# Kernel tuning notes

Measured on AMD Instinct MI355X. Metric: run time of the kernel, lower is better.

The kernel has to match this reference:

```python
import jax, jax.numpy as jnp
import numpy as np


def _warp(x, flow):
    """Bilinear backward warp (grid_sample, zeros padding, pixel coords).
    x: [B,C,H,W], flow: [B,2,H,W] with flow[:,0]=dx, flow[:,1]=dy."""
    B, C, H, W = x.shape
    gx = jnp.arange(W, dtype=x.dtype)[None, None, :] + flow[:, 0]  # [B,H,W]
    gy = jnp.arange(H, dtype=x.dtype)[None, :, None] + flow[:, 1]  # [B,H,W]
    x0 = jnp.floor(gx)
    y0 = jnp.floor(gy)
    wx = gx - x0
    wy = gy - y0
    x0 = x0.astype(jnp.int32)
    y0 = y0.astype(jnp.int32)
    xf = x.reshape(B, C, H * W)

    def tap(yi, xi, w):
        valid = (xi >= 0) & (xi < W) & (yi >= 0) & (yi < H)
        idx = (jnp.clip(yi, 0, H - 1) * W + jnp.clip(xi, 0, W - 1)).reshape(B, 1, H * W)
        v = jnp.take_along_axis(xf, idx, axis=2).reshape(B, C, H, W)
        return v * (w * valid)[:, None]

    return (tap(y0, x0, (1 - wx) * (1 - wy))
            + tap(y0, x0 + 1, wx * (1 - wy))
            + tap(y0 + 1, x0, (1 - wx) * wy)
            + tap(y0 + 1, x0 + 1, wx * wy))


def _shift(flow, bias):
    # shift(Flow, motion): warp the flow field itself by a constant motion vector
    B, _, H, W = flow.shape
    const = jnp.broadcast_to(jnp.asarray(bias, flow.dtype).reshape(1, 2, 1, 1), (B, 2, H, W))
    return _warp(flow, const)


def _make_obmc(x, flow):
    vols = [_warp(x, flow)]
    for bias in ([0.0, 1.0], [1.0, 0.0], [0.0, -1.0], [-1.0, 0.0]):
        vols.append(_warp(x, _shift(flow, bias)))
    return jnp.concatenate(vols, axis=1)  # [B, 5*C, H, W]


def setup_inputs() -> dict:
    key = jax.random.key(0)
    k1, k2 = jax.random.split(key)
    x = jax.random.normal(k1, (4, 64, 256, 256), dtype=jnp.float32)
    flow = jax.random.normal(k2, (4, 2, 256, 256), dtype=jnp.float32) * 4.0
    return {"x": x, "flow": flow}


def reference(x, flow):
    return _make_obmc(x, flow)
```

## Files before the change

kernel.cpp:

```cpp
#include <hip/hip_runtime.h>

#define BB 4
#define CC 64
#define HH 256
#define WW 256
#define HWHW (HH * WW)

__global__ __launch_bounds__(256) void transpose_xk(const float* __restrict__ x,
                                                    float* __restrict__ xt) {
    __shared__ float tile[64][65];
    const int b = blockIdx.y;
    const int hw0 = blockIdx.x << 6;
    const int t = threadIdx.x;
    const float* xb = x + (size_t)b * CC * HWHW;

    const int cq = t >> 4;
    const int px4 = (t & 15) << 2;
#pragma unroll
    for (int k = 0; k < 4; ++k) {
        const int c = cq + (k << 4);
        const float4 v = *(const float4*)&xb[(size_t)c * HWHW + hw0 + px4];
        tile[c][px4 + 0] = v.x;
        tile[c][px4 + 1] = v.y;
        tile[c][px4 + 2] = v.z;
        tile[c][px4 + 3] = v.w;
    }
    __syncthreads();
    float* xtb = xt + ((size_t)b * HWHW << 6);
    const int hwq = t >> 4;
    const int c4 = (t & 15) << 2;
#pragma unroll
    for (int k = 0; k < 4; ++k) {
        const int hw = hwq + (k << 4);
        float4 v;
        v.x = tile[c4 + 0][hw];
        v.y = tile[c4 + 1][hw];
        v.z = tile[c4 + 2][hw];
        v.w = tile[c4 + 3][hw];
        *(float4*)&xtb[((size_t)(hw0 + hw) << 6) + c4] = v;
    }
}

__global__ __launch_bounds__(256) void obmc_kernel(const float* __restrict__ xt,
                                                   const float* __restrict__ flow,
                                                   float* __restrict__ out) {
    __shared__ int4 dOff[5][64];
    __shared__ float4 dW[5][64];
    __shared__ float sm[64][65];

    const int bid = ((blockIdx.x & 7) << 9) + (blockIdx.x >> 3);
    const int tx0 = (bid & 3) << 6;
    const int y = (bid >> 2) & 255;
    const int b = bid >> 10;
    const int t = threadIdx.x;
    const int wv = t >> 6;
    const int lane = t & 63;
    const int sp = lane >> 4;
    const int c4 = (lane & 15) << 2;

    const float* xtb = xt + ((size_t)b * HWHW << 6);
    const float* fb = flow + (size_t)b * 2 * HWHW;
    float* ob = out + (size_t)b * 5 * CC * HWHW + (size_t)y * WW + tx0;

    const int oys[5] = {0, 1, 0, -1, 0};
    const int oxs[5] = {0, 0, 1, 0, -1};

    for (int idx = t; idx < 320; idx += 256) {
        const int g = idx >> 6, px = idx & 63;
        const int sy = y + oys[g];
        const int sx = tx0 + px + oxs[g];
        float fx = 0.f, fy = 0.f;
        if ((unsigned)sy < HH && (unsigned)sx < WW) {
            const int fo = sy * WW + sx;
            fx = fb[fo];
            fy = fb[HWHW + fo];
        }
        const float gx = (float)(tx0 + px) + fx;
        const float gy = (float)y + fy;
        const float x0f = floorf(gx);
        const float y0f = floorf(gy);
        const float fwx = gx - x0f;
        const float fwy = gy - y0f;
        const int ix0 = (int)x0f, iy0 = (int)y0f;
        const int ix1 = ix0 + 1, iy1 = iy0 + 1;
        const float vx0 = ((unsigned)ix0 < WW) ? 1.f : 0.f;
        const float vx1 = ((unsigned)ix1 < WW) ? 1.f : 0.f;
        const float vy0 = ((unsigned)iy0 < HH) ? 1.f : 0.f;
        const float vy1 = ((unsigned)iy1 < HH) ? 1.f : 0.f;
        const int xc0 = min(max(ix0, 0), WW - 1);
        const int xc1 = min(max(ix1, 0), WW - 1);
        const int yc0 = min(max(iy0, 0), HH - 1);
        const int yc1 = min(max(iy1, 0), HH - 1);
        dOff[g][px] = make_int4((yc0 * WW + xc0) << 6, (yc0 * WW + xc1) << 6,
                                (yc1 * WW + xc0) << 6, (yc1 * WW + xc1) << 6);
        dW[g][px] = make_float4((1.f - fwx) * (1.f - fwy) * vx0 * vy0,
                                fwx * (1.f - fwy) * vx1 * vy0,
                                (1.f - fwx) * fwy * vx0 * vy1,
                                fwx * fwy * vx1 * vy1);
    }
    __syncthreads();

    for (int g = 0; g < 5; ++g) {
        float4 acc[4];
#pragma unroll
        for (int i = 0; i < 4; ++i) {
            const int px = (wv << 4) + (i << 2) + sp;
            const int4 o = dOff[g][px];
            const float4 w = dW[g][px];
            const float4 v0 = *(const float4*)(xtb + o.x + c4);
            const float4 v1 = *(const float4*)(xtb + o.y + c4);
            const float4 v2 = *(const float4*)(xtb + o.z + c4);
            const float4 v3 = *(const float4*)(xtb + o.w + c4);
            float4 a;
            a.x = w.x * v0.x; a.y = w.x * v0.y; a.z = w.x * v0.z; a.w = w.x * v0.w;
            a.x = fmaf(w.y, v1.x, a.x); a.y = fmaf(w.y, v1.y, a.y);
            a.z = fmaf(w.y, v1.z, a.z); a.w = fmaf(w.y, v1.w, a.w);
            a.x = fmaf(w.z, v2.x, a.x); a.y = fmaf(w.z, v2.y, a.y);
            a.z = fmaf(w.z, v2.z, a.z); a.w = fmaf(w.z, v2.w, a.w);
            a.x = fmaf(w.w, v3.x, a.x); a.y = fmaf(w.w, v3.y, a.y);
            a.z = fmaf(w.w, v3.z, a.z); a.w = fmaf(w.w, v3.w, a.w);
            acc[i] = a;
        }
#pragma unroll
        for (int i = 0; i < 4; ++i) {
            const int px = (wv << 4) + (i << 2) + sp;
            sm[c4 + 0][px] = acc[i].x;
            sm[c4 + 1][px] = acc[i].y;
            sm[c4 + 2][px] = acc[i].z;
            sm[c4 + 3][px] = acc[i].w;
        }
        __syncthreads();
#pragma unroll
        for (int k = 0; k < 16; ++k) {
            const int c = (wv << 4) + k;
            __builtin_nontemporal_store(sm[c][lane],
                                        &ob[(size_t)(g * CC + c) * HWHW + lane]);
        }
        __syncthreads();
    }
}

extern "C" void kernel_launch(void* const* d_in, const int* in_sizes, int n_in,
                              void* d_out, int out_size, void* d_ws, size_t ws_size,
                              hipStream_t stream) {
    const float* x = (const float*)d_in[0];
    const float* flow = (const float*)d_in[1];
    float* out = (float*)d_out;
    float* xt = (float*)d_ws;

    transpose_xk<<<dim3(HWHW / 64, BB), 256, 0, stream>>>(x, xt);
    obmc_kernel<<<BB * HH * (WW / 64), 256, 0, stream>>>(xt, flow, out);
}
```

Measured before the change: 411.9 us.

## Software-pipeline gather loads across groups with double-buffered shared tile

Unrolls the five-group loop and issues the gather loads for group g+1 before computing and storing group g, using two register buffers of 16 float4 each. The shared transpose tile is double-buffered, which removes the second barrier per group. The goal is to hide gather latency behind compute and stores, at the cost of much higher register pressure (32 float4 live values) that may lower occupancy.

```diff
diff --git a/kernel.cpp b/kernel.cpp
--- a/kernel.cpp
+++ b/kernel.cpp
@@ -46,7 +46,7 @@
                                                    float* __restrict__ out) {
     __shared__ int4 dOff[5][64];
     __shared__ float4 dW[5][64];
-    __shared__ float sm[64][65];
+    __shared__ float sm[2][64][65];
 
     const int bid = ((blockIdx.x & 7) << 9) + (blockIdx.x >> 3);
     const int tx0 = (bid & 3) << 6;
@@ -100,44 +100,65 @@
     }
     __syncthreads();
 
-    for (int g = 0; g < 5; ++g) {
-        float4 acc[4];
-#pragma unroll
-        for (int i = 0; i < 4; ++i) {
-            const int px = (wv << 4) + (i << 2) + sp;
-            const int4 o = dOff[g][px];
-            const float4 w = dW[g][px];
-            const float4 v0 = *(const float4*)(xtb + o.x + c4);
-            const float4 v1 = *(const float4*)(xtb + o.y + c4);
-            const float4 v2 = *(const float4*)(xtb + o.z + c4);
-            const float4 v3 = *(const float4*)(xtb + o.w + c4);
-            float4 a;
-            a.x = w.x * v0.x; a.y = w.x * v0.y; a.z = w.x * v0.z; a.w = w.x * v0.w;
-            a.x = fmaf(w.y, v1.x, a.x); a.y = fmaf(w.y, v1.y, a.y);
-            a.z = fmaf(w.y, v1.z, a.z); a.w = fmaf(w.y, v1.w, a.w);
-            a.x = fmaf(w.z, v2.x, a.x); a.y = fmaf(w.z, v2.y, a.y);
-            a.z = fmaf(w.z, v2.z, a.z); a.w = fmaf(w.z, v2.w, a.w);
-            a.x = fmaf(w.w, v3.x, a.x); a.y = fmaf(w.w, v3.y, a.y);
-            a.z = fmaf(w.w, v3.z, a.z); a.w = fmaf(w.w, v3.w, a.w);
-            acc[i] = a;
-        }
-#pragma unroll
-        for (int i = 0; i < 4; ++i) {
-            const int px = (wv << 4) + (i << 2) + sp;
-            sm[c4 + 0][px] = acc[i].x;
-            sm[c4 + 1][px] = acc[i].y;
-            sm[c4 + 2][px] = acc[i].z;
-            sm[c4 + 3][px] = acc[i].w;
-        }
-        __syncthreads();
-#pragma unroll
-        for (int k = 0; k < 16; ++k) {
-            const int c = (wv << 4) + k;
-            __builtin_nontemporal_store(sm[c][lane],
-                                        &ob[(size_t)(g * CC + c) * HWHW + lane]);
-        }
-        __syncthreads();
+    float4 va[16], vb[16];
+
+#define LOADG(G, DST)                                                          \
+    {                                                                          \
+        _Pragma("unroll") for (int i = 0; i < 4; ++i) {                        \
+            const int px = (wv << 4) + (i << 2) + sp;                          \
+            const int4 o = dOff[G][px];            \
+            DST[(i << 2) + 0] = *(const float4*)(xtb + o.x + c4);              \
+            DST[(i << 2) + 1] = *(const float4*)(xtb + o.y + c4);              \
+            DST[(i << 2) + 2] = *(const float4*)(xtb + o.z + c4);              \
+            DST[(i << 2) + 3] = *(const float4*)(xtb + o.w + c4);              \
+        }                                                                      \
     }
+
+#define GBODY(G, CUR, NXT, DO_NEXT)                                            \
+    {                                                                          \
+        if (DO_NEXT) LOADG((G) + 1, NXT);                                      \
+        _Pragma("unroll") for (int i = 0; i < 4; ++i) {                        \
+            const int px = (wv << 4) + (i << 2) + sp;                          \
+            const float4 w = dW[G][px];            \
+            float4 a;                                                          \
+            a.x = w.x * CUR[(i << 2)].x;                                       \
+            a.y = w.x * CUR[(i << 2)].y;                                       \
+            a.z = w.x * CUR[(i << 2)].z;                                       \
+            a.w = w.x * CUR[(i << 2)].w;                                       \
+            a.x = fmaf(w.y, CUR[(i << 2) + 1].x, a.x);                         \
+            a.y = fmaf(w.y, CUR[(i << 2) + 1].y, a.y);                         \
+            a.z = fmaf(w.y, CUR[(i << 2) + 1].z, a.z);                         \
+            a.w = fmaf(w.y, CUR[(i << 2) + 1].w, a.w);                         \
+            a.x = fmaf(w.z, CUR[(i << 2) + 2].x, a.x);                         \
+            a.y = fmaf(w.z, CUR[(i << 2) + 2].y, a.y);                         \
+            a.z = fmaf(w.z, CUR[(i << 2) + 2].z, a.z);                         \
+            a.w = fmaf(w.z, CUR[(i << 2) + 2].w, a.w);                         \
+            a.x = fmaf(w.w, CUR[(i << 2) + 3].x, a.x);                         \
+            a.y = fmaf(w.w, CUR[(i << 2) + 3].y, a.y);                         \
+            a.z = fmaf(w.w, CUR[(i << 2) + 3].z, a.z);                         \
+            a.w = fmaf(w.w, CUR[(i << 2) + 3].w, a.w);                         \
+            sm[(G) & 1][c4 + 0][px] = a.x;                                     \
+            sm[(G) & 1][c4 + 1][px] = a.y;                                     \
+            sm[(G) & 1][c4 + 2][px] = a.z;                                     \
+            sm[(G) & 1][c4 + 3][px] = a.w;                                     \
+        }                                                                      \
+        __syncthreads();                                                       \
+        _Pragma("unroll") for (int k = 0; k < 16; ++k) {                       \
+            const int c = (wv << 4) + k;                                       \
+            __builtin_nontemporal_store(                                       \
+                sm[(G) & 1][c][lane],                                          \
+                &ob[(size_t)((G)*CC + c) * HWHW + lane]);                      \
+        }                                                                      \
+    }
+
+    LOADG(0, va);
+    GBODY(0, va, vb, 1);
+    GBODY(1, vb, va, 1);
+    GBODY(2, va, vb, 1);
+    GBODY(3, vb, va, 1);
+    GBODY(4, va, vb, 0);
+#undef GBODY
+#undef LOADG
 }
 
 extern "C" void kernel_launch(void* const* d_in, const int* in_sizes, int n_in,
```

After: 420.3 us. 2.0% more time.
